# Optimization experiments

Hardware: AMD Instinct MI355X
Metric: run time of the kernel (lower is better)

The kernel has to match this reference:

```python
import jax, jax.numpy as jnp
import numpy as np

N_NODES = 100000
N_EDGES = 1600000
IN_FEATS = 128
HID = 128
OUT_FEATS = 64


def setup_inputs() -> dict:
    key = jax.random.key(0)
    ks = jax.random.split(key, 8)
    node_ids = jnp.arange(N_NODES, dtype=jnp.int64)
    src = jax.random.randint(ks[0], (N_EDGES,), 0, N_NODES, dtype=jnp.int64)
    dst = jax.random.randint(ks[1], (N_EDGES,), 0, N_NODES, dtype=jnp.int64)
    emb = jax.random.normal(ks[2], (N_NODES, IN_FEATS), dtype=jnp.float32)
    W1 = jax.random.normal(ks[3], (IN_FEATS, HID), dtype=jnp.float32) / np.sqrt(IN_FEATS)
    b1 = jnp.zeros((HID,), dtype=jnp.float32)
    W2 = jax.random.normal(ks[4], (HID, OUT_FEATS), dtype=jnp.float32) / np.sqrt(HID)
    b2 = jnp.zeros((OUT_FEATS,), dtype=jnp.float32)
    return {"node_ids": node_ids, "src": src, "dst": dst, "emb": emb,
            "W1": W1, "b1": b1, "W2": W2, "b2": b2}


def _sym_norms(src, dst):
    # DGL GraphConv norm='both': D_out^{-1/2} on source side, D_in^{-1/2} on dest side,
    # degrees clamped to >= 1.
    ones = jnp.ones(src.shape[0], dtype=jnp.float32)
    deg_out = jax.ops.segment_sum(ones, src, num_segments=N_NODES)
    deg_in = jax.ops.segment_sum(ones, dst, num_segments=N_NODES)
    norm_src = jnp.clip(deg_out, 1.0, None) ** -0.5  # [N]
    norm_dst = jnp.clip(deg_in, 1.0, None) ** -0.5   # [N]
    return norm_src, norm_dst


def _spmm(src, dst, h):
    # rst[dst] += h[src]  (sparse adjacency aggregation)
    return jax.ops.segment_sum(h[src], dst, num_segments=N_NODES)


def reference(node_ids, src, dst, emb, W1, b1, W2, b2):
    norm_src, norm_dst = _sym_norms(src, dst)
    h = emb[node_ids]                                   # [N, IN]
    # Layer 1 (IN -> HID, relu): weight applied after aggregation (in <= out)
    h = _spmm(src, dst, h * norm_src[:, None]) * norm_dst[:, None]
    h = jax.nn.relu(h @ W1 + b1)                        # [N, HID]
    # Dropout(0.5) is identity in eval mode.
    # Layer 2 (HID -> OUT): DGL applies weight BEFORE aggregation when in > out
    h = (h @ W2) * norm_src[:, None]                    # [N, OUT]
    h = _spmm(src, dst, h) * norm_dst[:, None] + b2
    return h
```

## Files before the change

### kernel.cpp

```cpp
#include <hip/hip_runtime.h>

#define N_N 100000
#define N_E 1600000
#define SLOTS 48
#define N_PAD 100096

#define BK_SHIFT 9
#define BK_SIZE 512
#define NBKT 196
#define MAXB 10240
#define EPB2 4096
#define NBLK2 ((N_E + EPB2 - 1) / EPB2)
#define EPT 16

#define BINC_BLKS (2 * NBKT)
#define EMB_BLKS 3125
#define W_BLKS 48

typedef unsigned short ushort_t;
typedef unsigned int uint_t;
typedef __bf16 bf16x8 __attribute__((ext_vector_type(8)));
typedef float f32x4 __attribute__((ext_vector_type(4)));

__device__ __forceinline__ ushort_t f2bf(float f) {
    uint_t u = __float_as_uint(f);
    u += 0x7fffu + ((u >> 16) & 1u);
    return (ushort_t)(u >> 16);
}

__device__ __forceinline__ uint_t pack_hl(float x) {
    uint_t xb = __float_as_uint(x);
    uint_t hb = (xb + 0x7fffu + ((xb >> 16) & 1u)) & 0xffff0000u;
    float rem = x - __uint_as_float(hb);
    uint_t rb = __float_as_uint(rem);
    uint_t lo = (rb + 0x7fffu + ((rb >> 16) & 1u)) >> 16;
    return (hb >> 16) | (lo << 16);
}

__device__ __forceinline__ bf16x8 as_bf16x8(uint4 u) {
    union { uint4 u; bf16x8 v; } c; c.u = u; return c.v;
}

__device__ __forceinline__ void unpack_frag(uint4 p0, uint4 p1, bf16x8& hi, bf16x8& lo) {
    uint4 h, l;
    h.x = (p0.x & 0xffffu) | (p0.y << 16);
    h.y = (p0.z & 0xffffu) | (p0.w << 16);
    h.z = (p1.x & 0xffffu) | (p1.y << 16);
    h.w = (p1.z & 0xffffu) | (p1.w << 16);
    l.x = (p0.x >> 16) | (p0.y & 0xffff0000u);
    l.y = (p0.z >> 16) | (p0.w & 0xffff0000u);
    l.z = (p1.x >> 16) | (p1.y & 0xffff0000u);
    l.w = (p1.z >> 16) | (p1.w & 0xffff0000u);
    hi = as_bf16x8(h); lo = as_bf16x8(l);
}

__global__ void __launch_bounds__(256) k_scatter(
        const int* __restrict__ src, const int* __restrict__ dst,
        int* __restrict__ cur_d, int* __restrict__ cur_s,
        uint_t* __restrict__ pe_dst, uint_t* __restrict__ pe_src) {
    __shared__ int hd[NBKT], hs[NBKT], od[NBKT], os_[NBKT];
    int t = threadIdx.x, blk = blockIdx.x;
    for (int i = t; i < NBKT; i += 256) { hd[i] = 0; hs[i] = 0; }
    __syncthreads();
    int e0 = blk * EPB2;
    int myS[EPT], myD[EPT];
    uint_t myR[EPT];
#pragma unroll
    for (int i = 0; i < EPT; i++) {
        int e = e0 + t + i * 256;
        if (e < N_E) {
            int s = src[e], d = dst[e];
            myS[i] = s; myD[i] = d;
            uint_t rd = (uint_t)atomicAdd(&hd[d >> BK_SHIFT], 1);
            uint_t rs = (uint_t)atomicAdd(&hs[s >> BK_SHIFT], 1);
            myR[i] = rd | (rs << 16);
        }
    }
    __syncthreads();
    for (int i = t; i < NBKT; i += 256) {
        int c = hd[i]; od[i]  = c ? atomicAdd(&cur_d[i], c) : 0;
        c = hs[i];     os_[i] = c ? atomicAdd(&cur_s[i], c) : 0;
    }
    __syncthreads();
#pragma unroll
    for (int i = 0; i < EPT; i++) {
        int e = e0 + t + i * 256;
        if (e < N_E) {
            int s = myS[i], d = myD[i];
            int rd = od[d >> BK_SHIFT] + (int)(myR[i] & 0xffffu);
            int rs = os_[s >> BK_SHIFT] + (int)(myR[i] >> 16);
            if (rd < MAXB) pe_dst[(size_t)(d >> BK_SHIFT) * MAXB + rd] =
                               (uint_t)s | ((uint_t)(d & 511) << 17);
            if (rs < MAXB) pe_src[(size_t)(s >> BK_SHIFT) * MAXB + rs] = (uint_t)s;
        }
    }
}

__global__ void __launch_bounds__(512) k_binC_prep(
        const uint_t* __restrict__ pe_dst, const uint_t* __restrict__ pe_src,
        const int* __restrict__ cur_d, const int* __restrict__ cur_s,
        int* __restrict__ slots, int* __restrict__ cnt,
        float* __restrict__ nd, float* __restrict__ ns,
        const float* __restrict__ emb, ushort_t* __restrict__ embb,
        const float* __restrict__ W1, const float* __restrict__ W2,
        uint_t* __restrict__ w1pk, uint_t* __restrict__ w2pk) {
    int t = threadIdx.x, bb = blockIdx.x;
    if (bb >= BINC_BLKS) {
        int pb = bb - BINC_BLKS;
        if (pb < EMB_BLKS) {
            int i = pb * 1024 + t;
            const float4* E4 = (const float4*)emb;
            ushort4* O4 = (ushort4*)embb;
            float4 v0 = E4[i], v1 = E4[i + 512];
            ushort4 o0, o1;
            o0.x = f2bf(v0.x); o0.y = f2bf(v0.y); o0.z = f2bf(v0.z); o0.w = f2bf(v0.w);
            o1.x = f2bf(v1.x); o1.y = f2bf(v1.y); o1.z = f2bf(v1.z); o1.w = f2bf(v1.w);
            O4[i] = o0; O4[i + 512] = o1;
        } else {
            int idx = (pb - EMB_BLKS) * 512 + t;
            int j = idx & 7, l = (idx >> 3) & 63;
            int k = (l >> 4) * 8 + j;
            int n = l & 15;
            if (idx < 16384) {
                int kc = (idx >> 9) & 3, nt = idx >> 11;
                w1pk[idx] = pack_hl(W1[(kc * 32 + k) * 128 + nt * 16 + n]);
            } else {
                int i2 = idx - 16384;
                int kc = (i2 >> 9) & 3, nt = i2 >> 11;
                w2pk[i2] = pack_hl(W2[(kc * 32 + k) * 64 + nt * 16 + n]);
            }
        }
        return;
    }
    __shared__ int lc[BK_SIZE];
    for (int i = t; i < BK_SIZE; i += 512) lc[i] = 0;
    __syncthreads();
    if (bb < NBKT) {
        int b = bb;
        int cb = min(cur_d[b], MAXB);
        int nbase = b << BK_SHIFT;
        const uint_t* pe = pe_dst + (size_t)b * MAXB;
        for (int e = t; e < cb; e += 512) {
            uint_t ed = pe[e];
            int dloc = (int)(ed >> 17);
            int s = (int)(ed & 0x1ffffu);
            int pos = atomicAdd(&lc[dloc], 1);
            if (pos < SLOTS) slots[(size_t)(nbase + dloc) * SLOTS + pos] = s;
        }
        __syncthreads();
        for (int i = t; i < BK_SIZE; i += 512) {
            int n = nbase + i;
            if (n < N_N) {
                int c = lc[i];
                cnt[n] = c;
                nd[n] = 1.0f / sqrtf((float)max(c, 1));
            }
        }
    } else {
        int b = bb - NBKT;
        int cb = min(cur_s[b], MAXB);
        int nbase = b << BK_SHIFT;
        const uint_t* pe = pe_src + (size_t)b * MAXB;
        for (int e = t; e < cb; e += 512)
            atomicAdd(&lc[(int)pe[e] - nbase], 1);
        __syncthreads();
        for (int i = t; i < BK_SIZE; i += 512) {
            int n = nbase + i;
            if (n < N_N) ns[n] = 1.0f / sqrtf((float)max(lc[i], 1));
        }
    }
}

__global__ void __launch_bounds__(256) k_spmm1(
        const int* __restrict__ cnt, const int* __restrict__ slots,
        const ushort_t* __restrict__ embb, const float* __restrict__ ns,
        const float* __restrict__ nd, uint_t* __restrict__ aggpk) {
    int wid = (blockIdx.x * 256 + (int)threadIdx.x) >> 6;
    int node = __builtin_amdgcn_readfirstlane(wid);
    if (node >= N_N) return;
    int lane = threadIdx.x & 63;
    const int* row = slots + node * SLOTS;
    int len = min(cnt[node], SLOTS);
    float ax0 = 0.f, ay0 = 0.f, ax1 = 0.f, ay1 = 0.f;
    int e = 0;
    int n8 = len & ~7;
    for (; e < n8; e += 8) {
        int s0 = __builtin_amdgcn_readfirstlane(row[e + 0]);
        int s1 = __builtin_amdgcn_readfirstlane(row[e + 1]);
        int s2 = __builtin_amdgcn_readfirstlane(row[e + 2]);
        int s3 = __builtin_amdgcn_readfirstlane(row[e + 3]);
        int s4 = __builtin_amdgcn_readfirstlane(row[e + 4]);
        int s5 = __builtin_amdgcn_readfirstlane(row[e + 5]);
        int s6 = __builtin_amdgcn_readfirstlane(row[e + 6]);
        int s7 = __builtin_amdgcn_readfirstlane(row[e + 7]);
        float w0 = ns[s0], w1 = ns[s1], w2 = ns[s2], w3 = ns[s3];
        float w4 = ns[s4], w5 = ns[s5], w6 = ns[s6], w7 = ns[s7];
        uint_t v0 = ((const uint_t*)(embb + (size_t)s0 * 128))[lane];
        uint_t v1 = ((const uint_t*)(embb + (size_t)s1 * 128))[lane];
        uint_t v2 = ((const uint_t*)(embb + (size_t)s2 * 128))[lane];
        uint_t v3 = ((const uint_t*)(embb + (size_t)s3 * 128))[lane];
        uint_t v4 = ((const uint_t*)(embb + (size_t)s4 * 128))[lane];
        uint_t v5 = ((const uint_t*)(embb + (size_t)s5 * 128))[lane];
        uint_t v6 = ((const uint_t*)(embb + (size_t)s6 * 128))[lane];
        uint_t v7 = ((const uint_t*)(embb + (size_t)s7 * 128))[lane];
        ax0 = fmaf(__uint_as_float(v0 << 16), w0, ax0);
        ay0 = fmaf(__uint_as_float(v0 & 0xffff0000u), w0, ay0);
        ax1 = fmaf(__uint_as_float(v1 << 16), w1, ax1);
        ay1 = fmaf(__uint_as_float(v1 & 0xffff0000u), w1, ay1);
        ax0 = fmaf(__uint_as_float(v2 << 16), w2, ax0);
        ay0 = fmaf(__uint_as_float(v2 & 0xffff0000u), w2, ay0);
        ax1 = fmaf(__uint_as_float(v3 << 16), w3, ax1);
        ay1 = fmaf(__uint_as_float(v3 & 0xffff0000u), w3, ay1);
        ax0 = fmaf(__uint_as_float(v4 << 16), w4, ax0);
        ay0 = fmaf(__uint_as_float(v4 & 0xffff0000u), w4, ay0);
        ax1 = fmaf(__uint_as_float(v5 << 16), w5, ax1);
        ay1 = fmaf(__uint_as_float(v5 & 0xffff0000u), w5, ay1);
        ax0 = fmaf(__uint_as_float(v6 << 16), w6, ax0);
        ay0 = fmaf(__uint_as_float(v6 & 0xffff0000u), w6, ay0);
        ax1 = fmaf(__uint_as_float(v7 << 16), w7, ax1);
        ay1 = fmaf(__uint_as_float(v7 & 0xffff0000u), w7, ay1);
    }
    int n4 = len & ~3;
    for (; e < n4; e += 4) {
        int s0 = __builtin_amdgcn_readfirstlane(row[e + 0]);
        int s1 = __builtin_amdgcn_readfirstlane(row[e + 1]);
        int s2 = __builtin_amdgcn_readfirstlane(row[e + 2]);
        int s3 = __builtin_amdgcn_readfirstlane(row[e + 3]);
        float w0 = ns[s0], w1 = ns[s1], w2 = ns[s2], w3 = ns[s3];
        uint_t v0 = ((const uint_t*)(embb + (size_t)s0 * 128))[lane];
        uint_t v1 = ((const uint_t*)(embb + (size_t)s1 * 128))[lane];
        uint_t v2 = ((const uint_t*)(embb + (size_t)s2 * 128))[lane];
        uint_t v3 = ((const uint_t*)(embb + (size_t)s3 * 128))[lane];
        ax0 = fmaf(__uint_as_float(v0 << 16), w0, ax0);
        ay0 = fmaf(__uint_as_float(v0 & 0xffff0000u), w0, ay0);
        ax1 = fmaf(__uint_as_float(v1 << 16), w1, ax1);
        ay1 = fmaf(__uint_as_float(v1 & 0xffff0000u), w1, ay1);
        ax0 = fmaf(__uint_as_float(v2 << 16), w2, ax0);
        ay0 = fmaf(__uint_as_float(v2 & 0xffff0000u), w2, ay0);
        ax1 = fmaf(__uint_as_float(v3 << 16), w3, ax1);
        ay1 = fmaf(__uint_as_float(v3 & 0xffff0000u), w3, ay1);
    }
    for (; e < len; ++e) {
        int s = __builtin_amdgcn_readfirstlane(row[e]);
        float w = ns[s];
        uint_t v = ((const uint_t*)(embb + (size_t)s * 128))[lane];
        ax0 = fmaf(__uint_as_float(v << 16), w, ax0);
        ay0 = fmaf(__uint_as_float(v & 0xffff0000u), w, ay0);
    }
    float sc = nd[node];
    uint2 o;
    o.x = pack_hl((ax0 + ax1) * sc);
    o.y = pack_hl((ay0 + ay1) * sc);
    ((uint2*)(aggpk + (size_t)node * 128))[lane] = o;
}

#define HST 140
__global__ void __launch_bounds__(256) k_gemm(
        const uint_t* __restrict__ aggpk, const uint_t* __restrict__ w1pk,
        const float* __restrict__ b1, const uint_t* __restrict__ w2pk,
        const float* __restrict__ ns, ushort_t* __restrict__ h2b) {
    __shared__ uint_t sh[64 * HST];
    int t = threadIdx.x;
    int w = t >> 6, l = t & 63;
    int quad = l >> 4, lm = l & 15;
    int nb0 = blockIdx.x * 64;

    f32x4 acc[8];
#pragma unroll
    for (int i = 0; i < 8; i++) acc[i] = (f32x4){0.f, 0.f, 0.f, 0.f};
    const uint_t* abase = aggpk + (size_t)(nb0 + w * 16 + lm) * 128 + quad * 8;
    bf16x8 ahi[4], alo[4];
#pragma unroll
    for (int kc = 0; kc < 4; kc++) {
        uint4 p0 = *(const uint4*)(abase + kc * 32);
        uint4 p1 = *(const uint4*)(abase + kc * 32 + 4);
        unpack_frag(p0, p1, ahi[kc], alo[kc]);
    }
#pragma unroll
    for (int nt = 0; nt < 8; nt++) {
#pragma unroll
        for (int kc = 0; kc < 4; kc++) {
            const uint_t* bb = w1pk + (((nt * 4 + kc) * 64 + l) << 3);
            uint4 q0 = *(const uint4*)(bb);
            uint4 q1 = *(const uint4*)(bb + 4);
            bf16x8 bhi, blo;
            unpack_frag(q0, q1, bhi, blo);
            acc[nt] = __builtin_amdgcn_mfma_f32_16x16x32_bf16(ahi[kc], bhi, acc[nt], 0, 0, 0);
            acc[nt] = __builtin_amdgcn_mfma_f32_16x16x32_bf16(ahi[kc], blo, acc[nt], 0, 0, 0);
            acc[nt] = __builtin_amdgcn_mfma_f32_16x16x32_bf16(alo[kc], bhi, acc[nt], 0, 0, 0);
        }
    }
#pragma unroll
    for (int nt = 0; nt < 8; nt++) {
        float bb = b1[nt * 16 + lm];
#pragma unroll
        for (int r = 0; r < 4; r++) {
            int row = w * 16 + quad * 4 + r;
            float hv = fmaxf(acc[nt][r] + bb, 0.f);
            sh[row * HST + nt * 16 + lm] = pack_hl(hv);
        }
    }
    __syncthreads();

    f32x4 acc2[4];
#pragma unroll
    for (int i = 0; i < 4; i++) acc2[i] = (f32x4){0.f, 0.f, 0.f, 0.f};
    const uint_t* sbase = sh + (w * 16 + lm) * HST + quad * 8;
    bf16x8 hhi[4], hlo[4];
#pragma unroll
    for (int kc = 0; kc < 4; kc++) {
        uint4 p0 = *(const uint4*)(sbase + kc * 32);
        uint4 p1 = *(const uint4*)(sbase + kc * 32 + 4);
        unpack_frag(p0, p1, hhi[kc], hlo[kc]);
    }
#pragma unroll
    for (int nt = 0; nt < 4; nt++) {
#pragma unroll
        for (int kc = 0; kc < 4; kc++) {
            const uint_t* bb = w2pk + (((nt * 4 + kc) * 64 + l) << 3);
            uint4 q0 = *(const uint4*)(bb);
            uint4 q1 = *(const uint4*)(bb + 4);
            bf16x8 bhi, blo;
            unpack_frag(q0, q1, bhi, blo);
            acc2[nt] = __builtin_amdgcn_mfma_f32_16x16x32_bf16(hhi[kc], bhi, acc2[nt], 0, 0, 0);
            acc2[nt] = __builtin_amdgcn_mfma_f32_16x16x32_bf16(hhi[kc], blo, acc2[nt], 0, 0, 0);
            acc2[nt] = __builtin_amdgcn_mfma_f32_16x16x32_bf16(hlo[kc], bhi, acc2[nt], 0, 0, 0);
        }
    }
#pragma unroll
    for (int r = 0; r < 4; r++) {
        int node = nb0 + w * 16 + quad * 4 + r;
        if (node < N_N) {
            float s = ns[node];
#pragma unroll
            for (int nt = 0; nt < 4; nt++)
                h2b[(size_t)node * 64 + nt * 16 + lm] = f2bf(acc2[nt][r] * s);
        }
    }
}

__global__ void __launch_bounds__(256) k_spmm2(
        const int* __restrict__ cnt, const int* __restrict__ slots,
        const ushort_t* __restrict__ h2b, const float* __restrict__ nd,
        const float* __restrict__ b2, float* __restrict__ out) {
    int wid = (blockIdx.x * 256 + (int)threadIdx.x) >> 6;
    int node = __builtin_amdgcn_readfirstlane(wid);
    if (node >= N_N) return;
    int lane = threadIdx.x & 63;
    int half = lane >> 5, w32 = lane & 31;
    const int* row = slots + node * SLOTS;
    int len = min(cnt[node], SLOTS);
    const uint_t* H = (const uint_t*)h2b;
    float a0 = 0.f, a1 = 0.f, b0 = 0.f, b1v = 0.f;
    int e = 0;
    int n8 = len & ~7;
    for (; e < n8; e += 8) {
        int i0 = e + half;
        int s0 = row[i0], s1 = row[i0 + 2], s2 = row[i0 + 4], s3 = row[i0 + 6];
        uint_t v0 = H[(size_t)s0 * 32 + w32];
        uint_t v1 = H[(size_t)s1 * 32 + w32];
        uint_t v2 = H[(size_t)s2 * 32 + w32];
        uint_t v3 = H[(size_t)s3 * 32 + w32];
        a0 += __uint_as_float(v0 << 16); a1 += __uint_as_float(v0 & 0xffff0000u);
        b0 += __uint_as_float(v1 << 16); b1v += __uint_as_float(v1 & 0xffff0000u);
        a0 += __uint_as_float(v2 << 16); a1 += __uint_as_float(v2 & 0xffff0000u);
        b0 += __uint_as_float(v3 << 16); b1v += __uint_as_float(v3 & 0xffff0000u);
    }
    for (; e + 1 < len; e += 2) {
        int s = row[e + half];
        uint_t v = H[(size_t)s * 32 + w32];
        a0 += __uint_as_float(v << 16); a1 += __uint_as_float(v & 0xffff0000u);
    }
    if (e < len && half == 0) {
        int s = row[e];
        uint_t v = H[(size_t)s * 32 + w32];
        a0 += __uint_as_float(v << 16); a1 += __uint_as_float(v & 0xffff0000u);
    }
    a0 += b0; a1 += b1v;
    a0 += __shfl_xor(a0, 32);
    a1 += __shfl_xor(a1, 32);
    if (half == 0) {
        float sc = nd[node];
        float2 bb = ((const float2*)b2)[w32];
        float2 o;
        o.x = a0 * sc + bb.x;
        o.y = a1 * sc + bb.y;
        ((float2*)(out + (size_t)node * 64))[w32] = o;
    }
}

extern "C" void kernel_launch(void* const* d_in, const int* in_sizes, int n_in,
                              void* d_out, int out_size, void* d_ws, size_t ws_size,
                              hipStream_t stream) {
    const int* src = (const int*)d_in[1];
    const int* dst = (const int*)d_in[2];
    const float* emb = (const float*)d_in[3];
    const float* W1 = (const float*)d_in[4];
    const float* b1 = (const float*)d_in[5];
    const float* W2 = (const float*)d_in[6];
    const float* b2 = (const float*)d_in[7];
    float* out = (float*)d_out;

    int* cur_d   = (int*)d_ws;
    int* cur_s   = cur_d + 256;
    int* cnt     = cur_s + 256;
    float* ns    = (float*)(cnt + N_PAD);
    float* nd    = ns + N_PAD;
    int* slots   = (int*)(nd + N_PAD);
    uint_t* pe_dst = (uint_t*)(slots + (size_t)N_N * SLOTS);
    uint_t* pe_src = pe_dst + (size_t)NBKT * MAXB;
    ushort_t* embb = (ushort_t*)(pe_src + (size_t)NBKT * MAXB);
    uint_t* aggpk = (uint_t*)(embb + (size_t)N_PAD * 128);
    uint_t* w1pk = aggpk + (size_t)N_PAD * 128;
    uint_t* w2pk = w1pk + 16384;
    ushort_t* h2b = (ushort_t*)(w2pk + 8192);

    hipMemsetAsync(cur_d, 0, sizeof(int) * 512, stream);
    k_scatter  <<<NBLK2, 256, 0, stream>>>(src, dst, cur_d, cur_s, pe_dst, pe_src);
    k_binC_prep<<<BINC_BLKS + EMB_BLKS + W_BLKS, 512, 0, stream>>>(
        pe_dst, pe_src, cur_d, cur_s, slots, cnt, nd, ns, emb, embb, W1, W2, w1pk, w2pk);
    k_spmm1 <<<(N_N + 3) / 4, 256, 0, stream>>>(cnt, slots, embb, ns, nd, aggpk);
    k_gemm  <<<(N_N + 63) / 64, 256, 0, stream>>>(aggpk, w1pk, b1, w2pk, ns, h2b);
    k_spmm2 <<<(N_N + 3) / 4, 256, 0, stream>>>(cnt, slots, h2b, nd, b2, out);
}
```

Measured before the change: 320.6 us.

## Fuse layer-1 SpMM aggregation into the GEMM kernel via shared memory

Merges the first sparse aggregation kernel into the dense GEMM kernel. Each 64-node block now gathers its neighbour rows per wave into shared memory and runs the MFMA layer-1/layer-2 GEMMs straight from LDS. This drops the round trip of the packed aggregation buffer through global memory and one kernel launch. In exchange, each wave walks 16 nodes one after another, which means fewer concurrent waves for the gather. That may expose more latency in the memory-bound gather phase. An extra barrier is added before the shared buffer is reused.

```diff
diff --git a/kernel.cpp b/kernel.cpp
--- a/kernel.cpp
+++ b/kernel.cpp
@@ -171,104 +171,105 @@
     }
 }
 
-__global__ void __launch_bounds__(256) k_spmm1(
+#define HST 140
+__global__ void __launch_bounds__(256) k_fused(
         const int* __restrict__ cnt, const int* __restrict__ slots,
         const ushort_t* __restrict__ embb, const float* __restrict__ ns,
-        const float* __restrict__ nd, uint_t* __restrict__ aggpk) {
-    int wid = (blockIdx.x * 256 + (int)threadIdx.x) >> 6;
-    int node = __builtin_amdgcn_readfirstlane(wid);
-    if (node >= N_N) return;
-    int lane = threadIdx.x & 63;
-    const int* row = slots + node * SLOTS;
-    int len = min(cnt[node], SLOTS);
-    float ax0 = 0.f, ay0 = 0.f, ax1 = 0.f, ay1 = 0.f;
-    int e = 0;
-    int n8 = len & ~7;
-    for (; e < n8; e += 8) {
-        int s0 = __builtin_amdgcn_readfirstlane(row[e + 0]);
-        int s1 = __builtin_amdgcn_readfirstlane(row[e + 1]);
-        int s2 = __builtin_amdgcn_readfirstlane(row[e + 2]);
-        int s3 = __builtin_amdgcn_readfirstlane(row[e + 3]);
-        int s4 = __builtin_amdgcn_readfirstlane(row[e + 4]);
-        int s5 = __builtin_amdgcn_readfirstlane(row[e + 5]);
-        int s6 = __builtin_amdgcn_readfirstlane(row[e + 6]);
-        int s7 = __builtin_amdgcn_readfirstlane(row[e + 7]);
-        float w0 = ns[s0], w1 = ns[s1], w2 = ns[s2], w3 = ns[s3];
-        float w4 = ns[s4], w5 = ns[s5], w6 = ns[s6], w7 = ns[s7];
-        uint_t v0 = ((const uint_t*)(embb + (size_t)s0 * 128))[lane];
-        uint_t v1 = ((const uint_t*)(embb + (size_t)s1 * 128))[lane];
-        uint_t v2 = ((const uint_t*)(embb + (size_t)s2 * 128))[lane];
-        uint_t v3 = ((const uint_t*)(embb + (size_t)s3 * 128))[lane];
-        uint_t v4 = ((const uint_t*)(embb + (size_t)s4 * 128))[lane];
-        uint_t v5 = ((const uint_t*)(embb + (size_t)s5 * 128))[lane];
-        uint_t v6 = ((const uint_t*)(embb + (size_t)s6 * 128))[lane];
-        uint_t v7 = ((const uint_t*)(embb + (size_t)s7 * 128))[lane];
-        ax0 = fmaf(__uint_as_float(v0 << 16), w0, ax0);
-        ay0 = fmaf(__uint_as_float(v0 & 0xffff0000u), w0, ay0);
-        ax1 = fmaf(__uint_as_float(v1 << 16), w1, ax1);
-        ay1 = fmaf(__uint_as_float(v1 & 0xffff0000u), w1, ay1);
-        ax0 = fmaf(__uint_as_float(v2 << 16), w2, ax0);
-        ay0 = fmaf(__uint_as_float(v2 & 0xffff0000u), w2, ay0);
-        ax1 = fmaf(__uint_as_float(v3 << 16), w3, ax1);
-        ay1 = fmaf(__uint_as_float(v3 & 0xffff0000u), w3, ay1);
-        ax0 = fmaf(__uint_as_float(v4 << 16), w4, ax0);
-        ay0 = fmaf(__uint_as_float(v4 & 0xffff0000u), w4, ay0);
-        ax1 = fmaf(__uint_as_float(v5 << 16), w5, ax1);
-        ay1 = fmaf(__uint_as_float(v5 & 0xffff0000u), w5, ay1);
-        ax0 = fmaf(__uint_as_float(v6 << 16), w6, ax0);
-        ay0 = fmaf(__uint_as_float(v6 & 0xffff0000u), w6, ay0);
-        ax1 = fmaf(__uint_as_float(v7 << 16), w7, ax1);
-        ay1 = fmaf(__uint_as_float(v7 & 0xffff0000u), w7, ay1);
-    }
-    int n4 = len & ~3;
-    for (; e < n4; e += 4) {
-        int s0 = __builtin_amdgcn_readfirstlane(row[e + 0]);
-        int s1 = __builtin_amdgcn_readfirstlane(row[e + 1]);
-        int s2 = __builtin_amdgcn_readfirstlane(row[e + 2]);
-        int s3 = __builtin_amdgcn_readfirstlane(row[e + 3]);
-        float w0 = ns[s0], w1 = ns[s1], w2 = ns[s2], w3 = ns[s3];
-        uint_t v0 = ((const uint_t*)(embb + (size_t)s0 * 128))[lane];
-        uint_t v1 = ((const uint_t*)(embb + (size_t)s1 * 128))[lane];
-        uint_t v2 = ((const uint_t*)(embb + (size_t)s2 * 128))[lane];
-        uint_t v3 = ((const uint_t*)(embb + (size_t)s3 * 128))[lane];
-        ax0 = fmaf(__uint_as_float(v0 << 16), w0, ax0);
-        ay0 = fmaf(__uint_as_float(v0 & 0xffff0000u), w0, ay0);
-        ax1 = fmaf(__uint_as_float(v1 << 16), w1, ax1);
-        ay1 = fmaf(__uint_as_float(v1 & 0xffff0000u), w1, ay1);
-        ax0 = fmaf(__uint_as_float(v2 << 16), w2, ax0);
-        ay0 = fmaf(__uint_as_float(v2 & 0xffff0000u), w2, ay0);
-        ax1 = fmaf(__uint_as_float(v3 << 16), w3, ax1);
-        ay1 = fmaf(__uint_as_float(v3 & 0xffff0000u), w3, ay1);
-    }
-    for (; e < len; ++e) {
-        int s = __builtin_amdgcn_readfirstlane(row[e]);
-        float w = ns[s];
-        uint_t v = ((const uint_t*)(embb + (size_t)s * 128))[lane];
-        ax0 = fmaf(__uint_as_float(v << 16), w, ax0);
-        ay0 = fmaf(__uint_as_float(v & 0xffff0000u), w, ay0);
-    }
-    float sc = nd[node];
-    uint2 o;
-    o.x = pack_hl((ax0 + ax1) * sc);
-    o.y = pack_hl((ay0 + ay1) * sc);
-    ((uint2*)(aggpk + (size_t)node * 128))[lane] = o;
-}
-
-#define HST 140
-__global__ void __launch_bounds__(256) k_gemm(
-        const uint_t* __restrict__ aggpk, const uint_t* __restrict__ w1pk,
+        const float* __restrict__ nd, const uint_t* __restrict__ w1pk,
         const float* __restrict__ b1, const uint_t* __restrict__ w2pk,
-        const float* __restrict__ ns, ushort_t* __restrict__ h2b) {
+        ushort_t* __restrict__ h2b) {
     __shared__ uint_t sh[64 * HST];
     int t = threadIdx.x;
     int w = t >> 6, l = t & 63;
     int quad = l >> 4, lm = l & 15;
     int nb0 = blockIdx.x * 64;
 
+    for (int i = 0; i < 16; i++) {
+        int ri = w * 16 + i;
+        int node = nb0 + ri;
+        float ax0 = 0.f, ay0 = 0.f, ax1 = 0.f, ay1 = 0.f;
+        float sc = 0.f;
+        if (node < N_N) {
+            const int* row = slots + (size_t)node * SLOTS;
+            int len = min(cnt[node], SLOTS);
+            int e = 0;
+            int n8 = len & ~7;
+            for (; e < n8; e += 8) {
+                int s0 = __builtin_amdgcn_readfirstlane(row[e + 0]);
+                int s1 = __builtin_amdgcn_readfirstlane(row[e + 1]);
+                int s2 = __builtin_amdgcn_readfirstlane(row[e + 2]);
+                int s3 = __builtin_amdgcn_readfirstlane(row[e + 3]);
+                int s4 = __builtin_amdgcn_readfirstlane(row[e + 4]);
+                int s5 = __builtin_amdgcn_readfirstlane(row[e + 5]);
+                int s6 = __builtin_amdgcn_readfirstlane(row[e + 6]);
+                int s7 = __builtin_amdgcn_readfirstlane(row[e + 7]);
+                float w0 = ns[s0], w1 = ns[s1], w2 = ns[s2], w3 = ns[s3];
+                float w4 = ns[s4], w5 = ns[s5], w6 = ns[s6], w7 = ns[s7];
+                uint_t v0 = ((const uint_t*)(embb + (size_t)s0 * 128))[l];
+                uint_t v1 = ((const uint_t*)(embb + (size_t)s1 * 128))[l];
+                uint_t v2 = ((const uint_t*)(embb + (size_t)s2 * 128))[l];
+                uint_t v3 = ((const uint_t*)(embb + (size_t)s3 * 128))[l];
+                uint_t v4 = ((const uint_t*)(embb + (size_t)s4 * 128))[l];
+                uint_t v5 = ((const uint_t*)(embb + (size_t)s5 * 128))[l];
+                uint_t v6 = ((const uint_t*)(embb + (size_t)s6 * 128))[l];
+                uint_t v7 = ((const uint_t*)(embb + (size_t)s7 * 128))[l];
+                ax0 = fmaf(__uint_as_float(v0 << 16), w0, ax0);
+                ay0 = fmaf(__uint_as_float(v0 & 0xffff0000u), w0, ay0);
+                ax1 = fmaf(__uint_as_float(v1 << 16), w1, ax1);
+                ay1 = fmaf(__uint_as_float(v1 & 0xffff0000u), w1, ay1);
+                ax0 = fmaf(__uint_as_float(v2 << 16), w2, ax0);
+                ay0 = fmaf(__uint_as_float(v2 & 0xffff0000u), w2, ay0);
+                ax1 = fmaf(__uint_as_float(v3 << 16), w3, ax1);
+                ay1 = fmaf(__uint_as_float(v3 & 0xffff0000u), w3, ay1);
+                ax0 = fmaf(__uint_as_float(v4 << 16), w4, ax0);
+                ay0 = fmaf(__uint_as_float(v4 & 0xffff0000u), w4, ay0);
+                ax1 = fmaf(__uint_as_float(v5 << 16), w5, ax1);
+                ay1 = fmaf(__uint_as_float(v5 & 0xffff0000u), w5, ay1);
+                ax0 = fmaf(__uint_as_float(v6 << 16), w6, ax0);
+                ay0 = fmaf(__uint_as_float(v6 & 0xffff0000u), w6, ay0);
+                ax1 = fmaf(__uint_as_float(v7 << 16), w7, ax1);
+                ay1 = fmaf(__uint_as_float(v7 & 0xffff0000u), w7, ay1);
+            }
+            int n4 = len & ~3;
+            for (; e < n4; e += 4) {
+                int s0 = __builtin_amdgcn_readfirstlane(row[e + 0]);
+                int s1 = __builtin_amdgcn_readfirstlane(row[e + 1]);
+                int s2 = __builtin_amdgcn_readfirstlane(row[e + 2]);
+                int s3 = __builtin_amdgcn_readfirstlane(row[e + 3]);
+                float w0 = ns[s0], w1 = ns[s1], w2 = ns[s2], w3 = ns[s3];
+                uint_t v0 = ((const uint_t*)(embb + (size_t)s0 * 128))[l];
+                uint_t v1 = ((const uint_t*)(embb + (size_t)s1 * 128))[l];
+                uint_t v2 = ((const uint_t*)(embb + (size_t)s2 * 128))[l];
+                uint_t v3 = ((const uint_t*)(embb + (size_t)s3 * 128))[l];
+                ax0 = fmaf(__uint_as_float(v0 << 16), w0, ax0);
+                ay0 = fmaf(__uint_as_float(v0 & 0xffff0000u), w0, ay0);
+                ax1 = fmaf(__uint_as_float(v1 << 16), w1, ax1);
+                ay1 = fmaf(__uint_as_float(v1 & 0xffff0000u), w1, ay1);
+                ax0 = fmaf(__uint_as_float(v2 << 16), w2, ax0);
+                ay0 = fmaf(__uint_as_float(v2 & 0xffff0000u), w2, ay0);
+                ax1 = fmaf(__uint_as_float(v3 << 16), w3, ax1);
+                ay1 = fmaf(__uint_as_float(v3 & 0xffff0000u), w3, ay1);
+            }
+            for (; e < len; ++e) {
+                int s = __builtin_amdgcn_readfirstlane(row[e]);
+                float wv = ns[s];
+                uint_t v = ((const uint_t*)(embb + (size_t)s * 128))[l];
+                ax0 = fmaf(__uint_as_float(v << 16), wv, ax0);
+                ay0 = fmaf(__uint_as_float(v & 0xffff0000u), wv, ay0);
+            }
+            sc = nd[node];
+        }
+        uint2 o;
+        o.x = pack_hl((ax0 + ax1) * sc);
+        o.y = pack_hl((ay0 + ay1) * sc);
+        *(uint2*)(sh + ri * HST + 2 * l) = o;
+    }
+    __syncthreads();
+
     f32x4 acc[8];
 #pragma unroll
     for (int i = 0; i < 8; i++) acc[i] = (f32x4){0.f, 0.f, 0.f, 0.f};
-    const uint_t* abase = aggpk + (size_t)(nb0 + w * 16 + lm) * 128 + quad * 8;
+    const uint_t* abase = sh + (w * 16 + lm) * HST + quad * 8;
     bf16x8 ahi[4], alo[4];
 #pragma unroll
     for (int kc = 0; kc < 4; kc++) {
@@ -290,6 +291,7 @@
             acc[nt] = __builtin_amdgcn_mfma_f32_16x16x32_bf16(alo[kc], bhi, acc[nt], 0, 0, 0);
         }
     }
+    __syncthreads();
 #pragma unroll
     for (int nt = 0; nt < 8; nt++) {
         float bb = b1[nt * 16 + lm];
@@ -410,8 +412,7 @@
     uint_t* pe_dst = (uint_t*)(slots + (size_t)N_N * SLOTS);
     uint_t* pe_src = pe_dst + (size_t)NBKT * MAXB;
     ushort_t* embb = (ushort_t*)(pe_src + (size_t)NBKT * MAXB);
-    uint_t* aggpk = (uint_t*)(embb + (size_t)N_PAD * 128);
-    uint_t* w1pk = aggpk + (size_t)N_PAD * 128;
+    uint_t* w1pk = (uint_t*)(embb + (size_t)N_PAD * 128);
     uint_t* w2pk = w1pk + 16384;
     ushort_t* h2b = (ushort_t*)(w2pk + 8192);
 
@@ -419,7 +420,6 @@
     k_scatter  <<<NBLK2, 256, 0, stream>>>(src, dst, cur_d, cur_s, pe_dst, pe_src);
     k_binC_prep<<<BINC_BLKS + EMB_BLKS + W_BLKS, 512, 0, stream>>>(
         pe_dst, pe_src, cur_d, cur_s, slots, cnt, nd, ns, emb, embb, W1, W2, w1pk, w2pk);
-    k_spmm1 <<<(N_N + 3) / 4, 256, 0, stream>>>(cnt, slots, embb, ns, nd, aggpk);
-    k_gemm  <<<(N_N + 63) / 64, 256, 0, stream>>>(aggpk, w1pk, b1, w2pk, ns, h2b);
+    k_fused <<<(N_N + 63) / 64, 256, 0, stream>>>(cnt, slots, embb, ns, nd, w1pk, b1, w2pk, h2b);
     k_spmm2 <<<(N_N + 3) / 4, 256, 0, stream>>>(cnt, slots, h2b, nd, b2, out);
 }
```

Result: slower. 351.6 us (+9.7%).

## Switch pipeline from split-bf16 hi/lo to plain fp16 with larger GEMM tiles

Applied to the files above, without the earlier changes.

Replaces the bf16 hi/lo split representation (three MFMAs per product) with single fp16 values for embeddings, aggregated features, weights and the layer-2 intermediate. This cuts the intermediate aggregate buffer in half, drops the unpack work and two thirds of the MFMAs. The GEMM kernel also processes 128 rows per block with reused B fragments. The cost is reduced precision and range: fp16 has fewer exponent bits than bf16 and is less accurate than the hi/lo split.

```diff
diff --git a/kernel.cpp b/kernel.cpp
--- a/kernel.cpp
+++ b/kernel.cpp
@@ -19,39 +19,23 @@
 
 typedef unsigned short ushort_t;
 typedef unsigned int uint_t;
-typedef __bf16 bf16x8 __attribute__((ext_vector_type(8)));
+typedef _Float16 f16x8 __attribute__((ext_vector_type(8)));
 typedef float f32x4 __attribute__((ext_vector_type(4)));
 
-__device__ __forceinline__ ushort_t f2bf(float f) {
-    uint_t u = __float_as_uint(f);
-    u += 0x7fffu + ((u >> 16) & 1u);
-    return (ushort_t)(u >> 16);
-}
-
-__device__ __forceinline__ uint_t pack_hl(float x) {
-    uint_t xb = __float_as_uint(x);
-    uint_t hb = (xb + 0x7fffu + ((xb >> 16) & 1u)) & 0xffff0000u;
-    float rem = x - __uint_as_float(hb);
-    uint_t rb = __float_as_uint(rem);
-    uint_t lo = (rb + 0x7fffu + ((rb >> 16) & 1u)) >> 16;
-    return (hb >> 16) | (lo << 16);
-}
-
-__device__ __forceinline__ bf16x8 as_bf16x8(uint4 u) {
-    union { uint4 u; bf16x8 v; } c; c.u = u; return c.v;
-}
-
-__device__ __forceinline__ void unpack_frag(uint4 p0, uint4 p1, bf16x8& hi, bf16x8& lo) {
-    uint4 h, l;
-    h.x = (p0.x & 0xffffu) | (p0.y << 16);
-    h.y = (p0.z & 0xffffu) | (p0.w << 16);
-    h.z = (p1.x & 0xffffu) | (p1.y << 16);
-    h.w = (p1.z & 0xffffu) | (p1.w << 16);
-    l.x = (p0.x >> 16) | (p0.y & 0xffff0000u);
-    l.y = (p0.z >> 16) | (p0.w & 0xffff0000u);
-    l.z = (p1.x >> 16) | (p1.y & 0xffff0000u);
-    l.w = (p1.z >> 16) | (p1.w & 0xffff0000u);
-    hi = as_bf16x8(h); lo = as_bf16x8(l);
+__device__ __forceinline__ ushort_t f2h(float f) {
+    union { _Float16 h; ushort_t u; } c; c.h = (_Float16)f; return c.u;
+}
+
+__device__ __forceinline__ void acc2h(uint_t v, float wv, float& a, float& b) {
+    union { uint_t u; _Float16 h[2]; } c; c.u = v;
+    a = fmaf((float)c.h[0], wv, a);
+    b = fmaf((float)c.h[1], wv, b);
+}
+
+__device__ __forceinline__ void addh(uint_t v, float& a, float& b) {
+    union { uint_t u; _Float16 h[2]; } c; c.u = v;
+    a += (float)c.h[0];
+    b += (float)c.h[1];
 }
 
 __global__ void __launch_bounds__(256) k_scatter(
@@ -101,20 +85,20 @@
         const int* __restrict__ cur_d, const int* __restrict__ cur_s,
         int* __restrict__ slots, int* __restrict__ cnt,
         float* __restrict__ nd, float* __restrict__ ns,
-        const float* __restrict__ emb, ushort_t* __restrict__ embb,
+        const float* __restrict__ emb, ushort_t* __restrict__ embf,
         const float* __restrict__ W1, const float* __restrict__ W2,
-        uint_t* __restrict__ w1pk, uint_t* __restrict__ w2pk) {
+        ushort_t* __restrict__ w1f, ushort_t* __restrict__ w2f) {
     int t = threadIdx.x, bb = blockIdx.x;
     if (bb >= BINC_BLKS) {
         int pb = bb - BINC_BLKS;
         if (pb < EMB_BLKS) {
             int i = pb * 1024 + t;
             const float4* E4 = (const float4*)emb;
-            ushort4* O4 = (ushort4*)embb;
+            ushort4* O4 = (ushort4*)embf;
             float4 v0 = E4[i], v1 = E4[i + 512];
             ushort4 o0, o1;
-            o0.x = f2bf(v0.x); o0.y = f2bf(v0.y); o0.z = f2bf(v0.z); o0.w = f2bf(v0.w);
-            o1.x = f2bf(v1.x); o1.y = f2bf(v1.y); o1.z = f2bf(v1.z); o1.w = f2bf(v1.w);
+            o0.x = f2h(v0.x); o0.y = f2h(v0.y); o0.z = f2h(v0.z); o0.w = f2h(v0.w);
+            o1.x = f2h(v1.x); o1.y = f2h(v1.y); o1.z = f2h(v1.z); o1.w = f2h(v1.w);
             O4[i] = o0; O4[i + 512] = o1;
         } else {
             int idx = (pb - EMB_BLKS) * 512 + t;
@@ -123,11 +107,11 @@
             int n = l & 15;
             if (idx < 16384) {
                 int kc = (idx >> 9) & 3, nt = idx >> 11;
-                w1pk[idx] = pack_hl(W1[(kc * 32 + k) * 128 + nt * 16 + n]);
+                w1f[idx] = f2h(W1[(kc * 32 + k) * 128 + nt * 16 + n]);
             } else {
                 int i2 = idx - 16384;
                 int kc = (i2 >> 9) & 3, nt = i2 >> 11;
-                w2pk[i2] = pack_hl(W2[(kc * 32 + k) * 64 + nt * 16 + n]);
+                w2f[i2] = f2h(W2[(kc * 32 + k) * 64 + nt * 16 + n]);
             }
         }
         return;
@@ -173,8 +157,8 @@
 
 __global__ void __launch_bounds__(256) k_spmm1(
         const int* __restrict__ cnt, const int* __restrict__ slots,
-        const ushort_t* __restrict__ embb, const float* __restrict__ ns,
-        const float* __restrict__ nd, uint_t* __restrict__ aggpk) {
+        const ushort_t* __restrict__ embf, const float* __restrict__ ns,
+        const float* __restrict__ nd, uint_t* __restrict__ aggf) {
     int wid = (blockIdx.x * 256 + (int)threadIdx.x) >> 6;
     int node = __builtin_amdgcn_readfirstlane(wid);
     if (node >= N_N) return;
@@ -195,30 +179,22 @@
         int s7 = __builtin_amdgcn_readfirstlane(row[e + 7]);
         float w0 = ns[s0], w1 = ns[s1], w2 = ns[s2], w3 = ns[s3];
         float w4 = ns[s4], w5 = ns[s5], w6 = ns[s6], w7 = ns[s7];
-        uint_t v0 = ((const uint_t*)(embb + (size_t)s0 * 128))[lane];
-        uint_t v1 = ((const uint_t*)(embb + (size_t)s1 * 128))[lane];
-        uint_t v2 = ((const uint_t*)(embb + (size_t)s2 * 128))[lane];
-        uint_t v3 = ((const uint_t*)(embb + (size_t)s3 * 128))[lane];
-        uint_t v4 = ((const uint_t*)(embb + (size_t)s4 * 128))[lane];
-        uint_t v5 = ((const uint_t*)(embb + (size_t)s5 * 128))[lane];
-        uint_t v6 = ((const uint_t*)(embb + (size_t)s6 * 128))[lane];
-        uint_t v7 = ((const uint_t*)(embb + (size_t)s7 * 128))[lane];
-        ax0 = fmaf(__uint_as_float(v0 << 16), w0, ax0);
-        ay0 = fmaf(__uint_as_float(v0 & 0xffff0000u), w0, ay0);
-        ax1 = fmaf(__uint_as_float(v1 << 16), w1, ax1);
-        ay1 = fmaf(__uint_as_float(v1 & 0xffff0000u), w1, ay1);
-        ax0 = fmaf(__uint_as_float(v2 << 16), w2, ax0);
-        ay0 = fmaf(__uint_as_float(v2 & 0xffff0000u), w2, ay0);
-        ax1 = fmaf(__uint_as_float(v3 << 16), w3, ax1);
-        ay1 = fmaf(__uint_as_float(v3 & 0xffff0000u), w3, ay1);
-        ax0 = fmaf(__uint_as_float(v4 << 16), w4, ax0);
-        ay0 = fmaf(__uint_as_float(v4 & 0xffff0000u), w4, ay0);
-        ax1 = fmaf(__uint_as_float(v5 << 16), w5, ax1);
-        ay1 = fmaf(__uint_as_float(v5 & 0xffff0000u), w5, ay1);
-        ax0 = fmaf(__uint_as_float(v6 << 16), w6, ax0);
-        ay0 = fmaf(__uint_as_float(v6 & 0xffff0000u), w6, ay0);
-        ax1 = fmaf(__uint_as_float(v7 << 16), w7, ax1);
-        ay1 = fmaf(__uint_as_float(v7 & 0xffff0000u), w7, ay1);
+        uint_t v0 = ((const uint_t*)(embf + (size_t)s0 * 128))[lane];
+        uint_t v1 = ((const uint_t*)(embf + (size_t)s1 * 128))[lane];
+        uint_t v2 = ((const uint_t*)(embf + (size_t)s2 * 128))[lane];
+        uint_t v3 = ((const uint_t*)(embf + (size_t)s3 * 128))[lane];
+        uint_t v4 = ((const uint_t*)(embf + (size_t)s4 * 128))[lane];
+        uint_t v5 = ((const uint_t*)(embf + (size_t)s5 * 128))[lane];
+        uint_t v6 = ((const uint_t*)(embf + (size_t)s6 * 128))[lane];
+        uint_t v7 = ((const uint_t*)(embf + (size_t)s7 * 128))[lane];
+        acc2h(v0, w0, ax0, ay0);
+        acc2h(v1, w1, ax1, ay1);
+        acc2h(v2, w2, ax0, ay0);
+        acc2h(v3, w3, ax1, ay1);
+        acc2h(v4, w4, ax0, ay0);
+        acc2h(v5, w5, ax1, ay1);
+        acc2h(v6, w6, ax0, ay0);
+        acc2h(v7, w7, ax1, ay1);
     }
     int n4 = len & ~3;
     for (; e < n4; e += 4) {
@@ -227,116 +203,116 @@
         int s2 = __builtin_amdgcn_readfirstlane(row[e + 2]);
         int s3 = __builtin_amdgcn_readfirstlane(row[e + 3]);
         float w0 = ns[s0], w1 = ns[s1], w2 = ns[s2], w3 = ns[s3];
-        uint_t v0 = ((const uint_t*)(embb + (size_t)s0 * 128))[lane];
-        uint_t v1 = ((const uint_t*)(embb + (size_t)s1 * 128))[lane];
-        uint_t v2 = ((const uint_t*)(embb + (size_t)s2 * 128))[lane];
-        uint_t v3 = ((const uint_t*)(embb + (size_t)s3 * 128))[lane];
-        ax0 = fmaf(__uint_as_float(v0 << 16), w0, ax0);
-        ay0 = fmaf(__uint_as_float(v0 & 0xffff0000u), w0, ay0);
-        ax1 = fmaf(__uint_as_float(v1 << 16), w1, ax1);
-        ay1 = fmaf(__uint_as_float(v1 & 0xffff0000u), w1, ay1);
-        ax0 = fmaf(__uint_as_float(v2 << 16), w2, ax0);
-        ay0 = fmaf(__uint_as_float(v2 & 0xffff0000u), w2, ay0);
-        ax1 = fmaf(__uint_as_float(v3 << 16), w3, ax1);
-        ay1 = fmaf(__uint_as_float(v3 & 0xffff0000u), w3, ay1);
+        uint_t v0 = ((const uint_t*)(embf + (size_t)s0 * 128))[lane];
+        uint_t v1 = ((const uint_t*)(embf + (size_t)s1 * 128))[lane];
+        uint_t v2 = ((const uint_t*)(embf + (size_t)s2 * 128))[lane];
+        uint_t v3 = ((const uint_t*)(embf + (size_t)s3 * 128))[lane];
+        acc2h(v0, w0, ax0, ay0);
+        acc2h(v1, w1, ax1, ay1);
+        acc2h(v2, w2, ax0, ay0);
+        acc2h(v3, w3, ax1, ay1);
     }
     for (; e < len; ++e) {
         int s = __builtin_amdgcn_readfirstlane(row[e]);
         float w = ns[s];
-        uint_t v = ((const uint_t*)(embb + (size_t)s * 128))[lane];
-        ax0 = fmaf(__uint_as_float(v << 16), w, ax0);
-        ay0 = fmaf(__uint_as_float(v & 0xffff0000u), w, ay0);
+        uint_t v = ((const uint_t*)(embf + (size_t)s * 128))[lane];
+        acc2h(v, w, ax0, ay0);
     }
     float sc = nd[node];
-    uint2 o;
-    o.x = pack_hl((ax0 + ax1) * sc);
-    o.y = pack_hl((ay0 + ay1) * sc);
-    ((uint2*)(aggpk + (size_t)node * 128))[lane] = o;
-}
-
-#define HST 140
-__global__ void __launch_bounds__(256) k_gemm(
-        const uint_t* __restrict__ aggpk, const uint_t* __restrict__ w1pk,
-        const float* __restrict__ b1, const uint_t* __restrict__ w2pk,
+    union { _Float16 h[2]; uint_t u; } p;
+    p.h[0] = (_Float16)((ax0 + ax1) * sc);
+    p.h[1] = (_Float16)((ay0 + ay1) * sc);
+    aggf[(size_t)node * 64 + lane] = p.u;
+}
+
+#define HSTH 136
+__global__ void __launch_bounds__(256, 2) k_gemm(
+        const ushort_t* __restrict__ aggf, const ushort_t* __restrict__ w1f,
+        const float* __restrict__ b1, const ushort_t* __restrict__ w2f,
         const float* __restrict__ ns, ushort_t* __restrict__ h2b) {
-    __shared__ uint_t sh[64 * HST];
+    __shared__ ushort_t sh[128 * HSTH];
     int t = threadIdx.x;
     int w = t >> 6, l = t & 63;
     int quad = l >> 4, lm = l & 15;
-    int nb0 = blockIdx.x * 64;
-
-    f32x4 acc[8];
-#pragma unroll
-    for (int i = 0; i < 8; i++) acc[i] = (f32x4){0.f, 0.f, 0.f, 0.f};
-    const uint_t* abase = aggpk + (size_t)(nb0 + w * 16 + lm) * 128 + quad * 8;
-    bf16x8 ahi[4], alo[4];
+    int nb0 = blockIdx.x * 128;
+
+    f16x8 a[2][4];
+#pragma unroll
+    for (int rt = 0; rt < 2; rt++)
+#pragma unroll
+        for (int kc = 0; kc < 4; kc++)
+            a[rt][kc] = *(const f16x8*)(aggf
+                + (size_t)(nb0 + rt * 64 + w * 16 + lm) * 128 + kc * 32 + quad * 8);
+
+    f32x4 acc[2][8];
+#pragma unroll
+    for (int rt = 0; rt < 2; rt++)
+#pragma unroll
+        for (int nt = 0; nt < 8; nt++) acc[rt][nt] = (f32x4){0.f, 0.f, 0.f, 0.f};
+
 #pragma unroll
     for (int kc = 0; kc < 4; kc++) {
-        uint4 p0 = *(const uint4*)(abase + kc * 32);
-        uint4 p1 = *(const uint4*)(abase + kc * 32 + 4);
-        unpack_frag(p0, p1, ahi[kc], alo[kc]);
-    }
-#pragma unroll
-    for (int nt = 0; nt < 8; nt++) {
-#pragma unroll
-        for (int kc = 0; kc < 4; kc++) {
-            const uint_t* bb = w1pk + (((nt * 4 + kc) * 64 + l) << 3);
-            uint4 q0 = *(const uint4*)(bb);
-            uint4 q1 = *(const uint4*)(bb + 4);
-            bf16x8 bhi, blo;
-            unpack_frag(q0, q1, bhi, blo);
-            acc[nt] = __builtin_amdgcn_mfma_f32_16x16x32_bf16(ahi[kc], bhi, acc[nt], 0, 0, 0);
-            acc[nt] = __builtin_amdgcn_mfma_f32_16x16x32_bf16(ahi[kc], blo, acc[nt], 0, 0, 0);
-            acc[nt] = __builtin_amdgcn_mfma_f32_16x16x32_bf16(alo[kc], bhi, acc[nt], 0, 0, 0);
+        f16x8 bq[8];
+#pragma unroll
+        for (int nt = 0; nt < 8; nt++)
+            bq[nt] = *(const f16x8*)(w1f + (((nt * 4 + kc) * 64 + l) << 3));
+#pragma unroll
+        for (int nt = 0; nt < 8; nt++) {
+            acc[0][nt] = __builtin_amdgcn_mfma_f32_16x16x32_f16(a[0][kc], bq[nt], acc[0][nt], 0, 0, 0);
+            acc[1][nt] = __builtin_amdgcn_mfma_f32_16x16x32_f16(a[1][kc], bq[nt], acc[1][nt], 0, 0, 0);
         }
     }
 #pragma unroll
     for (int nt = 0; nt < 8; nt++) {
         float bb = b1[nt * 16 + lm];
 #pragma unroll
+        for (int rt = 0; rt < 2; rt++)
+#pragma unroll
+            for (int r = 0; r < 4; r++) {
+                int row = rt * 64 + w * 16 + quad * 4 + r;
+                sh[row * HSTH + nt * 16 + lm] = f2h(fmaxf(acc[rt][nt][r] + bb, 0.f));
+            }
+    }
+    __syncthreads();
+
+    f16x8 h[2][4];
+#pragma unroll
+    for (int rt = 0; rt < 2; rt++)
+#pragma unroll
+        for (int kc = 0; kc < 4; kc++)
+            h[rt][kc] = *(const f16x8*)(sh + (rt * 64 + w * 16 + lm) * HSTH
+                                        + kc * 32 + quad * 8);
+
+    f32x4 acc2[2][4];
+#pragma unroll
+    for (int rt = 0; rt < 2; rt++)
+#pragma unroll
+        for (int q = 0; q < 4; q++) acc2[rt][q] = (f32x4){0.f, 0.f, 0.f, 0.f};
+
+#pragma unroll
+    for (int kc = 0; kc < 4; kc++) {
+        f16x8 b2q[4];
+#pragma unroll
+        for (int q = 0; q < 4; q++)
+            b2q[q] = *(const f16x8*)(w2f + (((q * 4 + kc) * 64 + l) << 3));
+#pragma unroll
+        for (int q = 0; q < 4; q++) {
+            acc2[0][q] = __builtin_amdgcn_mfma_f32_16x16x32_f16(h[0][kc], b2q[q], acc2[0][q], 0, 0, 0);
+            acc2[1][q] = __builtin_amdgcn_mfma_f32_16x16x32_f16(h[1][kc], b2q[q], acc2[1][q], 0, 0, 0);
+        }
+    }
+#pragma unroll
+    for (int rt = 0; rt < 2; rt++)
+#pragma unroll
         for (int r = 0; r < 4; r++) {
-            int row = w * 16 + quad * 4 + r;
-            float hv = fmaxf(acc[nt][r] + bb, 0.f);
-            sh[row * HST + nt * 16 + lm] = pack_hl(hv);
-        }
-    }
-    __syncthreads();
-
-    f32x4 acc2[4];
-#pragma unroll
-    for (int i = 0; i < 4; i++) acc2[i] = (f32x4){0.f, 0.f, 0.f, 0.f};
-    const uint_t* sbase = sh + (w * 16 + lm) * HST + quad * 8;
-    bf16x8 hhi[4], hlo[4];
-#pragma unroll
-    for (int kc = 0; kc < 4; kc++) {
-        uint4 p0 = *(const uint4*)(sbase + kc * 32);
-        uint4 p1 = *(const uint4*)(sbase + kc * 32 + 4);
-        unpack_frag(p0, p1, hhi[kc], hlo[kc]);
-    }
-#pragma unroll
-    for (int nt = 0; nt < 4; nt++) {
-#pragma unroll
-        for (int kc = 0; kc < 4; kc++) {
-            const uint_t* bb = w2pk + (((nt * 4 + kc) * 64 + l) << 3);
-            uint4 q0 = *(const uint4*)(bb);
-            uint4 q1 = *(const uint4*)(bb + 4);
-            bf16x8 bhi, blo;
-            unpack_frag(q0, q1, bhi, blo);
-            acc2[nt] = __builtin_amdgcn_mfma_f32_16x16x32_bf16(hhi[kc], bhi, acc2[nt], 0, 0, 0);
-            acc2[nt] = __builtin_amdgcn_mfma_f32_16x16x32_bf16(hhi[kc], blo, acc2[nt], 0, 0, 0);
-            acc2[nt] = __builtin_amdgcn_mfma_f32_16x16x32_bf16(hlo[kc], bhi, acc2[nt], 0, 0, 0);
-        }
-    }
-#pragma unroll
-    for (int r = 0; r < 4; r++) {
-        int node = nb0 + w * 16 + quad * 4 + r;
-        if (node < N_N) {
-            float s = ns[node];
-#pragma unroll
-            for (int nt = 0; nt < 4; nt++)
-                h2b[(size_t)node * 64 + nt * 16 + lm] = f2bf(acc2[nt][r] * s);
-        }
-    }
+            int node = nb0 + rt * 64 + w * 16 + quad * 4 + r;
+            if (node < N_N) {
+                float s = ns[node];
+#pragma unroll
+                for (int q = 0; q < 4; q++)
+                    h2b[(size_t)node * 64 + q * 16 + lm] = f2h(acc2[rt][q][r] * s);
+            }
+        }
 }
 
 __global__ void __launch_bounds__(256) k_spmm2(
@@ -361,20 +337,20 @@
         uint_t v1 = H[(size_t)s1 * 32 + w32];
         uint_t v2 = H[(size_t)s2 * 32 + w32];
         uint_t v3 = H[(size_t)s3 * 32 + w32];
-        a0 += __uint_as_float(v0 << 16); a1 += __uint_as_float(v0 & 0xffff0000u);
-        b0 += __uint_as_float(v1 << 16); b1v += __uint_as_float(v1 & 0xffff0000u);
-        a0 += __uint_as_float(v2 << 16); a1 += __uint_as_float(v2 & 0xffff0000u);
-        b0 += __uint_as_float(v3 << 16); b1v += __uint_as_float(v3 & 0xffff0000u);
+        addh(v0, a0, a1);
+        addh(v1, b0, b1v);
+        addh(v2, a0, a1);
+        addh(v3, b0, b1v);
     }
     for (; e + 1 < len; e += 2) {
         int s = row[e + half];
         uint_t v = H[(size_t)s * 32 + w32];
-        a0 += __uint_as_float(v << 16); a1 += __uint_as_float(v & 0xffff0000u);
+        addh(v, a0, a1);
     }
     if (e < len && half == 0) {
         int s = row[e];
         uint_t v = H[(size_t)s * 32 + w32];
-        a0 += __uint_as_float(v << 16); a1 += __uint_as_float(v & 0xffff0000u);
+        addh(v, a0, a1);
     }
     a0 += b0; a1 += b1v;
     a0 += __shfl_xor(a0, 32);
@@ -409,17 +385,17 @@
     int* slots   = (int*)(nd + N_PAD);
     uint_t* pe_dst = (uint_t*)(slots + (size_t)N_N * SLOTS);
     uint_t* pe_src = pe_dst + (size_t)NBKT * MAXB;
-    ushort_t* embb = (ushort_t*)(pe_src + (size_t)NBKT * MAXB);
-    uint_t* aggpk = (uint_t*)(embb + (size_t)N_PAD * 128);
-    uint_t* w1pk = aggpk + (size_t)N_PAD * 128;
-    uint_t* w2pk = w1pk + 16384;
-    ushort_t* h2b = (ushort_t*)(w2pk + 8192);
+    ushort_t* embf = (ushort_t*)(pe_src + (size_t)NBKT * MAXB);
+    uint_t* aggf = (uint_t*)(embf + (size_t)N_PAD * 128);
+    ushort_t* w1f = (ushort_t*)(aggf + (size_t)N_PAD * 64);
+    ushort_t* w2f = w1f + 16384;
+    ushort_t* h2b = w2f + 8192;
 
     hipMemsetAsync(cur_d, 0, sizeof(int) * 512, stream);
     k_scatter  <<<NBLK2, 256, 0, stream>>>(src, dst, cur_d, cur_s, pe_dst, pe_src);
     k_binC_prep<<<BINC_BLKS + EMB_BLKS + W_BLKS, 512, 0, stream>>>(
-        pe_dst, pe_src, cur_d, cur_s, slots, cnt, nd, ns, emb, embb, W1, W2, w1pk, w2pk);
-    k_spmm1 <<<(N_N + 3) / 4, 256, 0, stream>>>(cnt, slots, embb, ns, nd, aggpk);
-    k_gemm  <<<(N_N + 63) / 64, 256, 0, stream>>>(aggpk, w1pk, b1, w2pk, ns, h2b);
+        pe_dst, pe_src, cur_d, cur_s, slots, cnt, nd, ns, emb, embf, W1, W2, w1f, w2f);
+    k_spmm1 <<<(N_N + 3) / 4, 256, 0, stream>>>(cnt, slots, embf, ns, nd, aggf);
+    k_gemm  <<<N_PAD / 128, 256, 0, stream>>>((const ushort_t*)aggf, w1f, b1, w2f, ns, h2b);
     k_spmm2 <<<(N_N + 3) / 4, 256, 0, stream>>>(cnt, slots, h2b, nd, b2, out);
 }
```

Result: faster. 299.2 us (-6.7%).
